# Optimization experiments

Hardware: AMD Instinct MI355X
Metric: run time of the kernel (lower is better)

## Reference

```python
import jax, jax.numpy as jnp
import numpy as np

B, K, D = 8192, 8192, 512


def setup_inputs() -> dict:
    key = jax.random.key(0)
    k1, k2 = jax.random.split(key)
    previous_residual = jax.random.normal(k1, (B, D), dtype=jnp.float32)
    codebook_embeddings = jax.random.normal(k2, (K, D), dtype=jnp.float32)
    return {"previous_residual": previous_residual,
            "codebook_embeddings": codebook_embeddings}


def reference(previous_residual, codebook_embeddings):
    # Squared Euclidean distances [B, K] via the expansion
    # subtract+square+sum, without materializing the [B, K, D] intermediate).
    x_sq = jnp.sum(previous_residual * previous_residual, axis=-1, keepdims=True)   # [B, 1]
    e_sq = jnp.sum(codebook_embeddings * codebook_embeddings, axis=-1)              # [K]
    cross = jnp.einsum('bd,kd->bk', previous_residual, codebook_embeddings)         # [B, K]
    distances = x_sq - 2.0 * cross + e_sq[None, :]                                  # [B, K]
    closest_codebook_index = jnp.argmin(distances, axis=1)                          # [B] int
    codebook_embedding = codebook_embeddings[closest_codebook_index]                # [B, D] gather
    next_residual = previous_residual - codebook_embedding                          # [B, D]
    return closest_codebook_index, next_residual
```

## Files before the change

### kernel.cpp

```cpp
#include <hip/hip_runtime.h>

#define Bn 8192
#define Kn 8192
#define Dn 512
#define WINDOW 0.25f

typedef _Float16 half8 __attribute__((ext_vector_type(8)));
typedef float floatx4 __attribute__((ext_vector_type(4)));
typedef unsigned long long u64;

__device__ __forceinline__ unsigned int fkey(float f) {
    unsigned int u = __float_as_uint(f);
    return (u & 0x80000000u) ? ~u : (u | 0x80000000u);
}

__device__ __forceinline__ void gld16(const _Float16* g, _Float16* l) {
    __builtin_amdgcn_global_load_lds(
        (const __attribute__((address_space(1))) unsigned int*)g,
        (__attribute__((address_space(3))) unsigned int*)l, 16, 0, 0);
}

__global__ __launch_bounds__(256) void esq_kernel(const float* __restrict__ E,
                                                  float* __restrict__ esq) {
    int wave = threadIdx.x >> 6;
    int lane = threadIdx.x & 63;
    int k = blockIdx.x * 4 + wave;
    const float4* row = (const float4*)(E + (size_t)k * Dn);
    float4 v0 = row[lane];
    float4 v1 = row[64 + lane];
    float s = v0.x*v0.x + v0.y*v0.y + v0.z*v0.z + v0.w*v0.w
            + v1.x*v1.x + v1.y*v1.y + v1.z*v1.z + v1.w*v1.w;
    #pragma unroll
    for (int off = 32; off > 0; off >>= 1) s += __shfl_down(s, off, 64);
    if (lane == 0) esq[k] = s;
}

__global__ __launch_bounds__(256) void convert_hi(
    const float* __restrict__ X, const float* __restrict__ E,
    _Float16* __restrict__ Xh, _Float16* __restrict__ Eh,
    float* __restrict__ esq)
{
    const bool isE = blockIdx.x >= 1024;
    const int pc = blockIdx.x & 1023;
    const int panel = pc >> 4;
    const int chunk = pc & 15;
    const float* src = isE ? E : X;
    _Float16* dst = isE ? Eh : Xh;
    const int t = threadIdx.x;
    const int row = t >> 1;
    const int kh  = (t & 1) * 16;
    const float* p = &src[(size_t)(panel * 128 + row) * Dn + chunk * 32 + kh];
    float4 v[4];
    v[0] = *(const float4*)(p + 0);
    v[1] = *(const float4*)(p + 4);
    v[2] = *(const float4*)(p + 8);
    v[3] = *(const float4*)(p + 12);
    const int slotbase = ((row >> 6) << 8) + (((row >> 4) & 3) << 6) + (row & 15);
    #pragma unroll
    for (int j = 0; j < 2; ++j) {
        half8 h;
        #pragma unroll
        for (int q = 0; q < 2; ++q) {
            const float4 w = v[j * 2 + q];
            h[q*4+0]=(_Float16)w.x; h[q*4+1]=(_Float16)w.y;
            h[q*4+2]=(_Float16)w.z; h[q*4+3]=(_Float16)w.w;
        }
        const int kq = (t & 1) * 2 + j;
        const size_t off = ((size_t)(panel * 16 + chunk) * 512
                            + slotbase + kq * 16) * 8;
        *(half8*)&dst[off] = h;
    }
    if (isE) {
        float s = 0.f;
        #pragma unroll
        for (int i = 0; i < 4; ++i)
            s += v[i].x*v[i].x + v[i].y*v[i].y + v[i].z*v[i].z + v[i].w*v[i].w;
        s += __shfl_xor(s, 1);
        if ((t & 1) == 0) atomicAdd(&esq[panel * 128 + row], s);
    }
}

__global__ __launch_bounds__(512, 2) void argmin_hi(
    const _Float16* __restrict__ Xh, const _Float16* __restrict__ Eh,
    const float* __restrict__ esq, float* __restrict__ bestf)
{
    __shared__ __align__(16) _Float16 sA[2][2][2][4096];
    __shared__ __align__(16) _Float16 sB[2][2][2][4096];

    const int tid  = threadIdx.x;
    const int bid  = blockIdx.x;
    const int bx   = bid & 31;
    const int by   = bid >> 5;
    const int lane = tid & 63, wave = tid >> 6;
    const int wm   = wave >> 2;
    const int wn   = wave & 3;
    const int colg = lane & 15, quad = lane >> 4;

    const _Float16* gA = Xh + (size_t)(2 * by) * 65536 + tid * 8;
    const _Float16* gB = Eh + (size_t)(2 * bx) * 65536 + tid * 8;

    auto stgA = [&](int t, int kh, int b) {
        const int c = (2 * t + kh) * 4096;
        gld16(gA + c,         &sA[b][kh][0][tid * 8]);
        gld16(gA + 65536 + c, &sA[b][kh][1][tid * 8]);
    };
    auto stgB = [&](int t, int kh, int b) {
        const int c = (2 * t + kh) * 4096;
        gld16(gB + c,         &sB[b][kh][0][tid * 8]);
        gld16(gB + 65536 + c, &sB[b][kh][1][tid * 8]);
    };

    floatx4 acc[8][4];
    #pragma unroll
    for (int i = 0; i < 8; ++i)
        #pragma unroll
        for (int j = 0; j < 4; ++j) acc[i][j] = {0.f, 0.f, 0.f, 0.f};

    stgA(0, 0, 0); stgB(0, 0, 0); stgA(0, 1, 0); stgB(0, 1, 0);

    const int la8 = lane * 8;
    const int bo  = (wn & 1) * 2048 + la8;

    for (int t = 0; t < 8; ++t) {
        const int b = t & 1, nb = b ^ 1;
        const bool pf = (t < 7);
        const _Float16* A0 = &sA[b][0][wm][0];
        const _Float16* A1 = &sA[b][1][wm][0];
        const _Float16* B0 = &sB[b][0][wn >> 1][bo];
        const _Float16* B1 = &sB[b][1][wn >> 1][bo];
        half8 a[4], bb[4];

        asm volatile("s_waitcnt vmcnt(4)" ::: "memory");
        __builtin_amdgcn_s_barrier();

        #pragma unroll
        for (int ni = 0; ni < 4; ++ni) bb[ni] = *(const half8*)&B0[ni * 512];
        #pragma unroll
        for (int i = 0; i < 4; ++i)   a[i]  = *(const half8*)&A0[i * 512 + la8];
        if (pf) stgA(t + 1, 0, nb);
        __builtin_amdgcn_s_setprio(1);
        #pragma unroll
        for (int i = 0; i < 4; ++i)
            #pragma unroll
            for (int ni = 0; ni < 4; ++ni)
                acc[i][ni] = __builtin_amdgcn_mfma_f32_16x16x32_f16(
                    a[i], bb[ni], acc[i][ni], 0, 0, 0);
        __builtin_amdgcn_s_setprio(0);

        #pragma unroll
        for (int i = 0; i < 4; ++i) a[i] = *(const half8*)&A0[2048 + i * 512 + la8];
        if (pf) stgB(t + 1, 0, nb);
        __builtin_amdgcn_s_setprio(1);
        #pragma unroll
        for (int i = 0; i < 4; ++i)
            #pragma unroll
            for (int ni = 0; ni < 4; ++ni)
                acc[4 + i][ni] = __builtin_amdgcn_mfma_f32_16x16x32_f16(
                    a[i], bb[ni], acc[4 + i][ni], 0, 0, 0);
        __builtin_amdgcn_s_setprio(0);

        if (pf) asm volatile("s_waitcnt vmcnt(4)" ::: "memory");
        else    asm volatile("s_waitcnt vmcnt(0)" ::: "memory");
        __builtin_amdgcn_s_barrier();

        #pragma unroll
        for (int ni = 0; ni < 4; ++ni) bb[ni] = *(const half8*)&B1[ni * 512];
        #pragma unroll
        for (int i = 0; i < 4; ++i)   a[i]  = *(const half8*)&A1[i * 512 + la8];
        if (pf) stgA(t + 1, 1, nb);
        __builtin_amdgcn_s_setprio(1);
        #pragma unroll
        for (int i = 0; i < 4; ++i)
            #pragma unroll
            for (int ni = 0; ni < 4; ++ni)
                acc[i][ni] = __builtin_amdgcn_mfma_f32_16x16x32_f16(
                    a[i], bb[ni], acc[i][ni], 0, 0, 0);
        __builtin_amdgcn_s_setprio(0);

        #pragma unroll
        for (int i = 0; i < 4; ++i) a[i] = *(const half8*)&A1[2048 + i * 512 + la8];
        if (pf) stgB(t + 1, 1, nb);
        __builtin_amdgcn_s_setprio(1);
        #pragma unroll
        for (int i = 0; i < 4; ++i)
            #pragma unroll
            for (int ni = 0; ni < 4; ++ni)
                acc[4 + i][ni] = __builtin_amdgcn_mfma_f32_16x16x32_f16(
                    a[i], bb[ni], acc[4 + i][ni], 0, 0, 0);
        __builtin_amdgcn_s_setprio(0);
    }

    float2* sm = (float2*)&sA[0][0][0][0];
    const int n0 = bx * 256 + wn * 64;
    float eqv[4];
    #pragma unroll
    for (int ni = 0; ni < 4; ++ni) eqv[ni] = esq[n0 + ni * 16 + colg];
    const unsigned ob_base = ((unsigned)colg << 4) | ((unsigned)wn << 2);

    #pragma unroll
    for (int mi = 0; mi < 8; ++mi)
        #pragma unroll
        for (int r = 0; r < 4; ++r) {
            float w1 = INFINITY, w2 = INFINITY;
            #pragma unroll
            for (int ni = 0; ni < 4; ++ni) {
                const float dv = eqv[ni] - 2.0f * acc[mi][ni][r];
                const float key = __uint_as_float(
                    (__float_as_uint(dv) & 0xFFFFFF00u) | (ob_base | (unsigned)ni));
                w2 = fminf(w2, fmaxf(w1, key));
                w1 = fminf(w1, key);
            }
            #pragma unroll
            for (int off = 1; off < 16; off <<= 1) {
                const float p1 = __shfl_xor(w1, off);
                const float p2 = __shfl_xor(w2, off);
                w2 = fminf(fmaxf(w1, p1), fminf(w2, p2));
                w1 = fminf(w1, p1);
            }
            if (colg == 0) {
                const int row128 = mi * 16 + quad * 4 + r;
                float2 st; st.x = w1; st.y = w2;
                sm[(wm * 128 + row128) * 4 + wn] = st;
            }
        }
    __syncthreads();
    if (tid < 256) {
        float m1 = INFINITY, m2 = INFINITY;
        #pragma unroll
        for (int w = 0; w < 4; ++w) {
            const float2 p = sm[tid * 4 + w];
            m2 = fminf(fmaxf(m1, p.x), fminf(m2, p.y));
            m1 = fminf(m1, p.x);
        }
        float2 st; st.x = m1; st.y = m2;
        *(float2*)&bestf[(size_t)(by * 256 + tid) * 64 + bx * 2] = st;
    }
}

__global__ __launch_bounds__(256) void refine_kernel(
    const float* __restrict__ X, const float* __restrict__ E,
    const float* __restrict__ bestf, float* __restrict__ out)
{
    const int lane = threadIdx.x & 63, wave = threadIdx.x >> 6;
    const int b = blockIdx.x * 4 + wave;

    const float val = bestf[(size_t)b * 64 + lane];
    const unsigned bits = __float_as_uint(val);
    const int cb = lane >> 1;
    const int colg = (bits >> 4) & 15, wn = (bits >> 2) & 3, ni = bits & 3;
    const int col = cb * 256 + wn * 64 + ni * 16 + colg;

    float mn = val;
    #pragma unroll
    for (int off = 1; off < 64; off <<= 1) mn = fminf(mn, __shfl_xor(mn, off));

    const float4* xr = (const float4*)(X + (size_t)b * Dn);
    const float4 x0 = xr[lane * 2], x1 = xr[lane * 2 + 1];

    u64 bestk = ~0ull;
    u64 mask = __ballot(val <= mn + WINDOW);
    while (mask) {
        const int s = __builtin_ctzll(mask);
        mask &= mask - 1;
        const int c = __shfl(col, s);
        const float4* er = (const float4*)(E + (size_t)c * Dn);
        const float4 e0 = er[lane * 2], e1 = er[lane * 2 + 1];
        float p = e0.x*(e0.x - 2.f*x0.x) + e0.y*(e0.y - 2.f*x0.y)
                + e0.z*(e0.z - 2.f*x0.z) + e0.w*(e0.w - 2.f*x0.w)
                + e1.x*(e1.x - 2.f*x1.x) + e1.y*(e1.y - 2.f*x1.y)
                + e1.z*(e1.z - 2.f*x1.z) + e1.w*(e1.w - 2.f*x1.w);
        #pragma unroll
        for (int off = 1; off < 64; off <<= 1) p += __shfl_xor(p, off);
        const u64 k = ((u64)fkey(p) << 32) | (u64)(unsigned int)c;
        if (k < bestk) bestk = k;
    }

    const int idx = (int)(unsigned int)(bestk & 0xFFFFFFFFull);
    if (lane == 0) out[b] = (float)idx;
    const float4* er = (const float4*)(E + (size_t)idx * Dn);
    const float4 e0 = er[lane * 2], e1 = er[lane * 2 + 1];
    float4 r0, r1;
    r0.x = x0.x - e0.x; r0.y = x0.y - e0.y; r0.z = x0.z - e0.z; r0.w = x0.w - e0.w;
    r1.x = x1.x - e1.x; r1.y = x1.y - e1.y; r1.z = x1.z - e1.z; r1.w = x1.w - e1.w;
    float4* o = (float4*)(out + Bn + (size_t)b * Dn);
    o[lane * 2] = r0; o[lane * 2 + 1] = r1;
}

#define KSPLIT 16
#define LDSW 132
__global__ __launch_bounds__(256, 2) void argmin_fp32(
    const float* __restrict__ X, const float* __restrict__ E,
    const float* __restrict__ esq, u64* __restrict__ best)
{
    __shared__ __align__(16) float Xs[16][LDSW];
    __shared__ __align__(16) float Es[16][LDSW];
    __shared__ u64 red[128][16];
    const int tid = threadIdx.x;
    const int tx = tid & 15, ty = tid >> 4;
    const int rowTile = blockIdx.x / KSPLIT;
    const int split   = blockIdx.x % KSPLIT;
    const int m0 = rowTile * 128;
    const int kbase = split * (Kn / KSPLIT);
    float bestv[8]; int besti[8];
    #pragma unroll
    for (int i = 0; i < 8; ++i) { bestv[i] = INFINITY; besti[i] = 0; }
    const int ldRow = tid >> 2, ldD = (tid & 3) * 4;
    for (int kt = 0; kt < (Kn / KSPLIT) / 128; ++kt) {
        const int k0 = kbase + kt * 128;
        float acc[8][8] = {};
        for (int dc = 0; dc < Dn / 16; ++dc) {
            const int d0 = dc * 16;
            float4 xa = *(const float4*)&X[(size_t)(m0 + ldRow)      * Dn + d0 + ldD];
            float4 xb = *(const float4*)&X[(size_t)(m0 + 64 + ldRow) * Dn + d0 + ldD];
            float4 ea = *(const float4*)&E[(size_t)(k0 + ldRow)      * Dn + d0 + ldD];
            float4 eb = *(const float4*)&E[(size_t)(k0 + 64 + ldRow) * Dn + d0 + ldD];
            __syncthreads();
            Xs[ldD+0][ldRow] = xa.x; Xs[ldD+1][ldRow] = xa.y;
            Xs[ldD+2][ldRow] = xa.z; Xs[ldD+3][ldRow] = xa.w;
            Xs[ldD+0][64+ldRow] = xb.x; Xs[ldD+1][64+ldRow] = xb.y;
            Xs[ldD+2][64+ldRow] = xb.z; Xs[ldD+3][64+ldRow] = xb.w;
            Es[ldD+0][ldRow] = ea.x; Es[ldD+1][ldRow] = ea.y;
            Es[ldD+2][ldRow] = ea.z; Es[ldD+3][ldRow] = ea.w;
            Es[ldD+0][64+ldRow] = eb.x; Es[ldD+1][64+ldRow] = eb.y;
            Es[ldD+2][64+ldRow] = eb.z; Es[ldD+3][64+ldRow] = eb.w;
            __syncthreads();
            #pragma unroll
            for (int d = 0; d < 16; ++d) {
                float a8[8], b8[8];
                *(float4*)&a8[0] = *(const float4*)&Xs[d][4*ty];
                *(float4*)&a8[4] = *(const float4*)&Xs[d][64 + 4*ty];
                *(float4*)&b8[0] = *(const float4*)&Es[d][4*tx];
                *(float4*)&b8[4] = *(const float4*)&Es[d][64 + 4*tx];
                #pragma unroll
                for (int i = 0; i < 8; ++i)
                    #pragma unroll
                    for (int j = 0; j < 8; ++j) acc[i][j] += a8[i] * b8[j];
            }
        }
        #pragma unroll
        for (int j = 0; j < 8; ++j) {
            const int c = k0 + ((j < 4) ? (4*tx + j) : (64 + 4*tx + (j - 4)));
            const float eq = esq[c];
            #pragma unroll
            for (int i = 0; i < 8; ++i) {
                float dval = eq - 2.0f * acc[i][j];
                if (dval < bestv[i]) { bestv[i] = dval; besti[i] = c; }
            }
        }
    }
    #pragma unroll
    for (int i = 0; i < 8; ++i) {
        int rloc = (i < 4) ? (4*ty + i) : (64 + 4*ty + (i - 4));
        red[rloc][tx] = ((u64)fkey(bestv[i]) << 32) | (u64)(unsigned int)besti[i];
    }
    __syncthreads();
    if (tid < 128) {
        u64 m = red[tid][0];
        #pragma unroll
        for (int t = 1; t < 16; ++t) { u64 v = red[tid][t]; if (v < m) m = v; }
        best[(size_t)(m0 + tid) * KSPLIT + split] = m;
    }
}

__global__ __launch_bounds__(256) void finalize_kernel(
    const float* __restrict__ X, const float* __restrict__ E,
    const u64* __restrict__ best, float* __restrict__ out, int nsplits)
{
    __shared__ int sidx[2];
    const int half = threadIdx.x >> 7;
    const int t    = threadIdx.x & 127;
    const int b    = blockIdx.x * 2 + half;
    if (t < 64) {
        u64 v = (t < nsplits) ? best[(size_t)b * nsplits + t] : ~0ull;
        #pragma unroll
        for (int off = 1; off < 64; off <<= 1) {
            u64 o = __shfl_xor(v, off);
            if (o < v) v = o;
        }
        if (t == 0) {
            int idx = (int)(unsigned int)(v & 0xFFFFFFFFull);
            sidx[half] = idx;
            out[b] = (float)idx;
        }
    }
    __syncthreads();
    const int idx = sidx[half];
    float4 x = ((const float4*)(X + (size_t)b * Dn))[t];
    float4 e = ((const float4*)(E + (size_t)idx * Dn))[t];
    float4 r; r.x = x.x - e.x; r.y = x.y - e.y; r.z = x.z - e.z; r.w = x.w - e.w;
    ((float4*)(out + Bn + (size_t)b * Dn))[t] = r;
}

extern "C" void kernel_launch(void* const* d_in, const int* in_sizes, int n_in,
                              void* d_out, int out_size, void* d_ws, size_t ws_size,
                              hipStream_t stream) {
    const float* X = (const float*)d_in[0];
    const float* E = (const float*)d_in[1];
    float* out = (float*)d_out;

    const size_t HB = (size_t)Bn * Dn * sizeof(_Float16);
    const size_t BESTB = (size_t)Bn * 64 * sizeof(float);
    const size_t NEED = 32768 + 2 * HB + BESTB;

    float* esq = (float*)d_ws;

    if (ws_size >= NEED) {
        _Float16* Xh = (_Float16*)((char*)d_ws + 32768);
        _Float16* Eh = (_Float16*)((char*)d_ws + 32768 + HB);
        float* bestf = (float*)((char*)d_ws + 32768 + 2 * HB);
        hipMemsetAsync((void*)esq, 0, Kn * sizeof(float), stream);
        convert_hi<<<2048, 256, 0, stream>>>(X, E, Xh, Eh, esq);
        argmin_hi<<<1024, 512, 0, stream>>>(Xh, Eh, esq, bestf);
        refine_kernel<<<Bn / 4, 256, 0, stream>>>(X, E, bestf, out);
    } else {
        u64* best = (u64*)((char*)d_ws + 32768);
        esq_kernel<<<Kn / 4, 256, 0, stream>>>(E, esq);
        argmin_fp32<<<(Bn / 128) * KSPLIT, 256, 0, stream>>>(X, E, esq, best);
        finalize_kernel<<<Bn / 2, 256, 0, stream>>>(X, E, best, out, KSPLIT);
    }
}
```

Before: 179.0 us.

## Load codebook operand straight into registers, bypassing LDS staging

The codebook (B) tiles are no longer staged through shared memory. Each wave now loads its own B fragments directly from global memory into registers, double-buffered as bbA/bbB across the two K-halves of each step. The X tiles are still staged through LDS, with both halves prefetched together, which cuts the pipeline to one barrier per iteration and halves LDS use. In exchange, B loads are duplicated across the two wm waves and rely on L2 hits, and global-load latency has to be hidden behind the MFMAs.

```diff
diff --git a/kernel.cpp b/kernel.cpp
--- a/kernel.cpp
+++ b/kernel.cpp
@@ -85,7 +85,6 @@
     const float* __restrict__ esq, float* __restrict__ bestf)
 {
     __shared__ __align__(16) _Float16 sA[2][2][2][4096];
-    __shared__ __align__(16) _Float16 sB[2][2][2][4096];
 
     const int tid  = threadIdx.x;
     const int bid  = blockIdx.x;
@@ -95,20 +94,17 @@
     const int wm   = wave >> 2;
     const int wn   = wave & 3;
     const int colg = lane & 15, quad = lane >> 4;
+    const int la8  = lane * 8;
 
     const _Float16* gA = Xh + (size_t)(2 * by) * 65536 + tid * 8;
-    const _Float16* gB = Eh + (size_t)(2 * bx) * 65536 + tid * 8;
+    const _Float16* gB = Eh + (size_t)(2 * bx + (wn >> 1)) * 65536
+                            + (wn & 1) * 2048 + la8;
 
     auto stgA = [&](int t, int kh, int b) {
         const int c = (2 * t + kh) * 4096;
         gld16(gA + c,         &sA[b][kh][0][tid * 8]);
         gld16(gA + 65536 + c, &sA[b][kh][1][tid * 8]);
     };
-    auto stgB = [&](int t, int kh, int b) {
-        const int c = (2 * t + kh) * 4096;
-        gld16(gB + c,         &sB[b][kh][0][tid * 8]);
-        gld16(gB + 65536 + c, &sB[b][kh][1][tid * 8]);
-    };
 
     floatx4 acc[8][4];
     #pragma unroll
@@ -116,78 +112,59 @@
         #pragma unroll
         for (int j = 0; j < 4; ++j) acc[i][j] = {0.f, 0.f, 0.f, 0.f};
 
-    stgA(0, 0, 0); stgB(0, 0, 0); stgA(0, 1, 0); stgB(0, 1, 0);
-
-    const int la8 = lane * 8;
-    const int bo  = (wn & 1) * 2048 + la8;
+    half8 bbA[4], bbB[4];
+
+    stgA(0, 0, 0); stgA(0, 1, 0);
+    #pragma unroll
+    for (int ni = 0; ni < 4; ++ni)
+        bbA[ni] = *(const half8*)(gB + ni * 512);
+    asm volatile("s_waitcnt vmcnt(4)" ::: "memory");
+    __builtin_amdgcn_s_barrier();
 
     for (int t = 0; t < 8; ++t) {
         const int b = t & 1, nb = b ^ 1;
         const bool pf = (t < 7);
         const _Float16* A0 = &sA[b][0][wm][0];
         const _Float16* A1 = &sA[b][1][wm][0];
-        const _Float16* B0 = &sB[b][0][wn >> 1][bo];
-        const _Float16* B1 = &sB[b][1][wn >> 1][bo];
-        half8 a[4], bb[4];
-
-        asm volatile("s_waitcnt vmcnt(4)" ::: "memory");
-        __builtin_amdgcn_s_barrier();
-
-        #pragma unroll
-        for (int ni = 0; ni < 4; ++ni) bb[ni] = *(const half8*)&B0[ni * 512];
-        #pragma unroll
-        for (int i = 0; i < 4; ++i)   a[i]  = *(const half8*)&A0[i * 512 + la8];
-        if (pf) stgA(t + 1, 0, nb);
+        half8 a[8];
+
+        #pragma unroll
+        for (int ni = 0; ni < 4; ++ni)
+            bbB[ni] = *(const half8*)(gB + (2 * t + 1) * 4096 + ni * 512);
+        #pragma unroll
+        for (int j = 0; j < 8; ++j)
+            a[j] = *(const half8*)&A0[(j >> 2) * 2048 + (j & 3) * 512 + la8];
         __builtin_amdgcn_s_setprio(1);
         #pragma unroll
-        for (int i = 0; i < 4; ++i)
+        for (int j = 0; j < 8; ++j)
             #pragma unroll
             for (int ni = 0; ni < 4; ++ni)
-                acc[i][ni] = __builtin_amdgcn_mfma_f32_16x16x32_f16(
-                    a[i], bb[ni], acc[i][ni], 0, 0, 0);
+                acc[j][ni] = __builtin_amdgcn_mfma_f32_16x16x32_f16(
+                    a[j], bbA[ni], acc[j][ni], 0, 0, 0);
         __builtin_amdgcn_s_setprio(0);
 
-        #pragma unroll
-        for (int i = 0; i < 4; ++i) a[i] = *(const half8*)&A0[2048 + i * 512 + la8];
-        if (pf) stgB(t + 1, 0, nb);
+        if (pf) {
+            stgA(t + 1, 0, nb); stgA(t + 1, 1, nb);
+            #pragma unroll
+            for (int ni = 0; ni < 4; ++ni)
+                bbA[ni] = *(const half8*)(gB + (2 * t + 2) * 4096 + ni * 512);
+        }
+        #pragma unroll
+        for (int j = 0; j < 8; ++j)
+            a[j] = *(const half8*)&A1[(j >> 2) * 2048 + (j & 3) * 512 + la8];
         __builtin_amdgcn_s_setprio(1);
         #pragma unroll
-        for (int i = 0; i < 4; ++i)
+        for (int j = 0; j < 8; ++j)
             #pragma unroll
             for (int ni = 0; ni < 4; ++ni)
-                acc[4 + i][ni] = __builtin_amdgcn_mfma_f32_16x16x32_f16(
-                    a[i], bb[ni], acc[4 + i][ni], 0, 0, 0);
+                acc[j][ni] = __builtin_amdgcn_mfma_f32_16x16x32_f16(
+                    a[j], bbB[ni], acc[j][ni], 0, 0, 0);
         __builtin_amdgcn_s_setprio(0);
 
-        if (pf) asm volatile("s_waitcnt vmcnt(4)" ::: "memory");
-        else    asm volatile("s_waitcnt vmcnt(0)" ::: "memory");
-        __builtin_amdgcn_s_barrier();
-
-        #pragma unroll
-        for (int ni = 0; ni < 4; ++ni) bb[ni] = *(const half8*)&B1[ni * 512];
-        #pragma unroll
-        for (int i = 0; i < 4; ++i)   a[i]  = *(const half8*)&A1[i * 512 + la8];
-        if (pf) stgA(t + 1, 1, nb);
-        __builtin_amdgcn_s_setprio(1);
-        #pragma unroll
-        for (int i = 0; i < 4; ++i)
-            #pragma unroll
-            for (int ni = 0; ni < 4; ++ni)
-                acc[i][ni] = __builtin_amdgcn_mfma_f32_16x16x32_f16(
-                    a[i], bb[ni], acc[i][ni], 0, 0, 0);
-        __builtin_amdgcn_s_setprio(0);
-
-        #pragma unroll
-        for (int i = 0; i < 4; ++i) a[i] = *(const half8*)&A1[2048 + i * 512 + la8];
-        if (pf) stgB(t + 1, 1, nb);
-        __builtin_amdgcn_s_setprio(1);
-        #pragma unroll
-        for (int i = 0; i < 4; ++i)
-            #pragma unroll
-            for (int ni = 0; ni < 4; ++ni)
-                acc[4 + i][ni] = __builtin_amdgcn_mfma_f32_16x16x32_f16(
-                    a[i], bb[ni], acc[4 + i][ni], 0, 0, 0);
-        __builtin_amdgcn_s_setprio(0);
+        if (pf) {
+            asm volatile("s_waitcnt vmcnt(4)" ::: "memory");
+            __builtin_amdgcn_s_barrier();
+        }
     }
 
     float2* sm = (float2*)&sA[0][0][0][0];
```

Measured after the change: 178.6 us. Within noise of the previous version (-0.2%).
